# Performance work log

Hardware: AMD Instinct MI355X
Metric: run time of the kernel (lower is better)

## Reference

```python
import jax, jax.numpy as jnp
import numpy as np

N_LAYERS = 4
NA = 64    # n_processor_a
NB = 64    # n_processor_b
NP = NA + NB
M = 32     # N_modes
HA = 512   # fine grid resolution
HB = 128   # coarse grid resolution
N_IN_A = 4
N_IN_B = 4
N_OUT_A = 2


def setup_inputs() -> dict:
    key = jax.random.key(0)
    ks = jax.random.split(key, 16)
    def w(k, shape, fan_in):
        return jax.random.normal(k, shape, jnp.float32) * (fan_in ** -0.5)
    return {
        "u_a": jax.random.normal(ks[0], (2, HA, HA), jnp.float32),
        "x_a": jax.random.normal(ks[1], (2, HA, HA), jnp.float32),
        "u_b": jax.random.normal(ks[2], (2, HB, HB), jnp.float32),
        "x_b": jax.random.normal(ks[3], (2, HB, HB), jnp.float32),
        "enc_a_w": w(ks[4], (NA, N_IN_A), N_IN_A),
        "enc_a_b": jnp.zeros((NA,), jnp.float32),
        "enc_b_w": w(ks[5], (NB, N_IN_B), N_IN_B),
        "enc_b_b": jnp.zeros((NB,), jnp.float32),
        "dec_w": w(ks[6], (N_OUT_A, NA), NA),
        "dec_b": jnp.zeros((N_OUT_A,), jnp.float32),
        "c1a_w": w(ks[7], (N_LAYERS, NA, NA), NA),
        "c1a_b": jnp.zeros((N_LAYERS, NA), jnp.float32),
        "c2a_w": w(ks[8], (N_LAYERS, NA, NA), NA),
        "c2a_b": jnp.zeros((N_LAYERS, NA), jnp.float32),
        "c1b_w": w(ks[9], (N_LAYERS - 1, NB, NB), NB),
        "c1b_b": jnp.zeros((N_LAYERS - 1, NB), jnp.float32),
        "c2b_w": w(ks[10], (N_LAYERS - 1, NB, NB), NB),
        "c2b_b": jnp.zeros((N_LAYERS - 1, NB), jnp.float32),
        "A_re": jax.random.normal(ks[11], (N_LAYERS, NP, NP, M, M), jnp.float32) * 0.02,
        "A_im": jax.random.normal(ks[12], (N_LAYERS, NP, NP, M, M), jnp.float32) * 0.02,
    }


def conv1x1(w, b, x):
    # w: [out,in], b: [out], x: [in,H,W] -> [out,H,W]
    return jnp.einsum('oi,ihw->ohw', w, x) + b[:, None, None]


def rfft2_truncate(x, m):
    # x: [C,H,W] real -> [C,m,m] complex (forward-normalized, centered rows)
    c = jnp.fft.rfft2(x, norm='forward')[:, :, :m]
    return jnp.roll(c, m // 2, axis=1)[:, :m]


def irfft2_pad(c, m, s):
    # c: [C,m,m] complex -> [C,*s] real
    c = jnp.pad(c, ((0, 0), (0, s[0] - c.shape[1]), (0, s[1] - c.shape[2])))
    c = jnp.roll(c, -(m // 2), axis=1)
    return jnp.fft.irfft2(c, s=s, norm='forward')


def biscale_spectral_conv(ua, ub, Wc):
    m = Wc.shape[-1]
    coeff = jnp.concatenate([rfft2_truncate(ua, m), rfft2_truncate(ub, m)], axis=0)
    coeff = jnp.einsum('oimn,imn->omn', Wc, coeff)  # complex channel mixing per mode
    na = ua.shape[0]
    out1 = irfft2_pad(coeff[:na], m, ua.shape[1:])
    out2 = irfft2_pad(coeff[na:], m, ub.shape[1:])
    return out1, out2


def _forward(u_a, x_a, u_b, x_b, enc_a_w, enc_a_b, enc_b_w, enc_b_b, dec_w, dec_b,
             c1a_w, c1a_b, c2a_w, c2a_b, c1b_w, c1b_b, c2b_w, c2b_b, A_re, A_im):
    A = A_re + 1j * A_im  # [L, NP, NP, M, M] complex64
    ua = conv1x1(enc_a_w, enc_a_b, jnp.concatenate([x_a, u_a], 0))
    ub = conv1x1(enc_b_w, enc_b_b, jnp.concatenate([x_b, u_b], 0))
    n_layers_b = c1b_w.shape[0]
    for i in range(A.shape[0]):
        ua_, ub_ = biscale_spectral_conv(ua, ub, A[i])
        ua = ua + jax.nn.gelu(conv1x1(c2a_w[i], c2a_b[i],
                                      jax.nn.gelu(conv1x1(c1a_w[i], c1a_b[i], ua_))))
        if i != n_layers_b:
            ub = ub + jax.nn.gelu(conv1x1(c2b_w[i], c2b_b[i],
                                          jax.nn.gelu(conv1x1(c1b_w[i], c1b_b[i], ub_))))
    ua = conv1x1(dec_w, dec_b, ua)
    return (ua, ub)


def reference(u_a, x_a, u_b, x_b, enc_a_w, enc_a_b, enc_b_w, enc_b_b, dec_w, dec_b,
              c1a_w, c1a_b, c2a_w, c2a_b, c1b_w, c1b_b, c2b_w, c2b_b, A_re, A_im):
    return _forward(u_a, x_a, u_b, x_b, enc_a_w, enc_a_b, enc_b_w, enc_b_b, dec_w, dec_b,
                    c1a_w, c1a_b, c2a_w, c2a_b, c1b_w, c1b_b, c2b_w, c2b_b, A_re, A_im)
```

## Files before the change

kernel.cpp:

```cpp
#include <hip/hip_runtime.h>
#include <hip/hip_bf16.h>
#include <math.h>


__device__ __forceinline__ float gelu_f(float x) {
  float t = tanhf(0.7978845608028654f * (x + 0.044715f * x * x * x));
  return 0.5f * x * (1.0f + t);
}

__device__ __forceinline__ float2 cmulf(float2 a, float2 b) {
  return make_float2(a.x * b.x - a.y * b.y, a.x * b.y + a.y * b.x);
}

__global__ void ktab(float2* __restrict__ t512) {
  int k = blockIdx.x * 256 + threadIdx.x;
  if (k < 512) {
    float a = (float)((double)k * (6.283185307179586 / 512.0));
    t512[k] = make_float2(cosf(a), sinf(a));
  }
}

template <int HW>
__global__ __launch_bounds__(256) void kenc(const float* __restrict__ xin,
                                            const float* __restrict__ uin,
                                            const float* __restrict__ w,
                                            const float* __restrict__ b,
                                            float* __restrict__ out) {
  int p = blockIdx.x * 256 + threadIdx.x;
  float i0 = xin[p], i1 = xin[HW + p];
  float i2 = uin[p], i3 = uin[HW + p];
  for (int c = 0; c < 64; ++c)
    out[(size_t)c * HW + p] =
        w[c * 4 + 0] * i0 + w[c * 4 + 1] * i1 + w[c * 4 + 2] * i2 + w[c * 4 + 3] * i3 + b[c];
}

template <int H, int MUL>
__global__ __launch_bounds__(256) void kfwd1(const float* __restrict__ x, float2* __restrict__ G,
                                             const float2* __restrict__ tw, float fs) {
  constexpr int PAD = H + 8;
  __shared__ float sm[8 * PAD];
  int c = blockIdx.x / (H / 8);
  int h8 = blockIdx.x % (H / 8);
  const float* src = x + ((size_t)c * H + h8 * 8) * H;
  for (int i = threadIdx.x; i < 2 * H; i += 256) {
    float4 g = ((const float4*)src)[i];
    int r = (i * 4) >> (H == 512 ? 9 : 7);
    int col = (i * 4) & (H - 1);
    *(float4*)&sm[r * PAD + col] = g;
  }
  __syncthreads();
  int kc = threadIdx.x >> 3;
  int hl = threadIdx.x & 7;
  float2 w0 = tw[(kc * MUL) & 511];
  float twoc = 2.f * w0.x;
  const float* row = sm + hl * PAD;
  float v1 = 0.f, v2 = 0.f;
#pragma unroll 4
  for (int w = 0; w < H; w += 2) {
    v2 = fmaf(twoc, v1, row[w] - v2);
    v1 = fmaf(twoc, v2, row[w + 1] - v1);
  }
  int h = h8 * 8 + hl;
  G[((size_t)c * 32 + kc) * H + h] =
      make_float2(fs * fmaf(w0.x, v1, -v2), fs * (w0.y * v1));
}

template <int H, int MUL>
__global__ __launch_bounds__(256) void kfwd2(const float2* __restrict__ G, float2* __restrict__ coeff,
                                             const float2* __restrict__ tw, int cbase) {
  __shared__ float2 gs[H];
  int c = blockIdx.x >> 5, kc = blockIdx.x & 31;
  const float2* gr = G + ((size_t)c * 32 + kc) * H;
  for (int i = threadIdx.x; i < H; i += 256) gs[i] = gr[i];
  __syncthreads();
  int jr = threadIdx.x >> 3, sub = threadIdx.x & 7;
  int f = jr - 16;
  float2 cur = tw[(f * sub * MUL) & 511];
  float2 step = tw[(f * 8 * MUL) & 511];
  float re = 0.f, im = 0.f;
  for (int j = 0; j < H / 8; ++j) {
    float2 g = gs[sub + 8 * j];
    re += g.x * cur.x + g.y * cur.y;
    im += g.y * cur.x - g.x * cur.y;
    cur = cmulf(cur, step);
  }
  for (int d = 1; d < 8; d <<= 1) {
    re += __shfl_down(re, d, 8);
    im += __shfl_down(im, d, 8);
  }
  if (sub == 0) coeff[(size_t)(cbase + c) * 1024 + jr * 32 + kc] = make_float2(re, im);
}

__global__ __launch_bounds__(256) void kmix(const float* __restrict__ Are,
                                            const float* __restrict__ Aim,
                                            const float2* __restrict__ cin,
                                            float2* __restrict__ cout) {
  int idx = blockIdx.x * 256 + threadIdx.x;
  int mn = idx & 1023;
  int o = idx >> 10;
  const float* ar = Are + (size_t)o * 131072 + mn;
  const float* ai = Aim + (size_t)o * 131072 + mn;
  float re = 0.f, im = 0.f;
  for (int i = 0; i < 128; ++i) {
    float wr = ar[(size_t)i * 1024];
    float wi = ai[(size_t)i * 1024];
    float2 x = cin[(size_t)i * 1024 + mn];
    re += wr * x.x - wi * x.y;
    im += wr * x.y + wi * x.x;
  }
  cout[(size_t)o * 1024 + mn] = make_float2(re, im);
}

template <int H, int MUL>
__global__ __launch_bounds__(256) void kinv1(const float2* __restrict__ coeff, float2* __restrict__ T,
                                             const float2* __restrict__ tw, int cbase) {
  __shared__ float2 cs[1024];
  int c = blockIdx.x / (H / 8);
  int h8 = blockIdx.x % (H / 8);
  const float2* cr = coeff + (size_t)(cbase + c) * 1024;
  for (int i = threadIdx.x; i < 1024; i += 256) cs[i] = cr[i];
  __syncthreads();
  int kc = threadIdx.x & 31;
  int hl = threadIdx.x >> 5;
  int h = h8 * 8 + hl;
  float2 cur = tw[((-16) * h * MUL) & 511];
  float2 step = tw[(h * MUL) & 511];
  float re = 0.f, im = 0.f;
  for (int jr = 0; jr < 32; ++jr) {
    float2 x = cs[jr * 32 + kc];
    re += x.x * cur.x - x.y * cur.y;
    im += x.x * cur.y + x.y * cur.x;
    cur = cmulf(cur, step);
  }
  float wgt = (kc == 0) ? 1.f : 2.f;
  T[((size_t)c * H + h) * 32 + kc] = make_float2(re * wgt, im * wgt);
}

template <int H, int MUL, int RPB>
__global__ __launch_bounds__(256) void kinv2(const float2* __restrict__ T, float* __restrict__ out,
                                             const float2* __restrict__ tw) {
  constexpr int QW = H / 4;
  __shared__ float2 ts[RPB * 32];
  size_t row0 = (size_t)blockIdx.x * RPB;
  for (int i = threadIdx.x; i < RPB * 32; i += 256) ts[i] = T[row0 * 32 + i];
  __syncthreads();
  int r = threadIdx.x / QW;
  int w0 = threadIdx.x % QW;
  float2 b = tw[(w0 * MUL) & 511];
  float2 c = make_float2(1.f, 0.f);
  float a0 = 0.f, a1 = 0.f, a2 = 0.f, a3 = 0.f;
  const float2* tr = &ts[r * 32];
#pragma unroll
  for (int kc = 0; kc < 32; kc += 4) {
    float2 t0 = tr[kc];
    float zre = t0.x * c.x - t0.y * c.y;
    a0 += zre; a1 += zre; a2 += zre; a3 += zre;
    c = cmulf(c, b);
    t0 = tr[kc + 1];
    zre = t0.x * c.x - t0.y * c.y;
    float zim = t0.x * c.y + t0.y * c.x;
    a0 += zre; a1 -= zim; a2 -= zre; a3 += zim;
    c = cmulf(c, b);
    t0 = tr[kc + 2];
    zre = t0.x * c.x - t0.y * c.y;
    a0 += zre; a1 -= zre; a2 += zre; a3 -= zre;
    c = cmulf(c, b);
    t0 = tr[kc + 3];
    zre = t0.x * c.x - t0.y * c.y;
    zim = t0.x * c.y + t0.y * c.x;
    a0 += zre; a1 += zim; a2 -= zre; a3 -= zim;
    c = cmulf(c, b);
  }
  float* orow = out + (row0 + r) * H + w0;
  orow[0] = a0;
  orow[QW] = a1;
  orow[2 * QW] = a2;
  orow[3 * QW] = a3;
}

template <int HW>
__global__ __launch_bounds__(256) void kconv(const float* __restrict__ xin, float* __restrict__ uio,
                                             const float* __restrict__ w1, const float* __restrict__ b1,
                                             const float* __restrict__ w2, const float* __restrict__ b2) {
  __shared__ float Xs[64][65];
  __shared__ float Ws[64][65];
  int p0 = blockIdx.x * 64;
  int t = threadIdx.x;
  for (int i = t; i < 4096; i += 256) {
    int r = i >> 6, cidx = i & 63;
    Xs[r][cidx] = xin[(size_t)r * HW + p0 + cidx];
    Ws[r][cidx] = w1[i];
  }
  __syncthreads();
  int ocb = (t >> 4) * 4;
  int pb = (t & 15) * 4;
  float acc[16];
#pragma unroll
  for (int i = 0; i < 4; ++i) {
    float bi = b1[ocb + i];
#pragma unroll
    for (int j = 0; j < 4; ++j) acc[i * 4 + j] = bi;
  }
  for (int ci = 0; ci < 64; ++ci) {
    float a0 = Ws[ocb + 0][ci], a1 = Ws[ocb + 1][ci], a2 = Ws[ocb + 2][ci], a3 = Ws[ocb + 3][ci];
    float x0 = Xs[ci][pb + 0], x1 = Xs[ci][pb + 1], x2 = Xs[ci][pb + 2], x3 = Xs[ci][pb + 3];
    acc[0] = fmaf(a0, x0, acc[0]); acc[1] = fmaf(a0, x1, acc[1]);
    acc[2] = fmaf(a0, x2, acc[2]); acc[3] = fmaf(a0, x3, acc[3]);
    acc[4] = fmaf(a1, x0, acc[4]); acc[5] = fmaf(a1, x1, acc[5]);
    acc[6] = fmaf(a1, x2, acc[6]); acc[7] = fmaf(a1, x3, acc[7]);
    acc[8] = fmaf(a2, x0, acc[8]); acc[9] = fmaf(a2, x1, acc[9]);
    acc[10] = fmaf(a2, x2, acc[10]); acc[11] = fmaf(a2, x3, acc[11]);
    acc[12] = fmaf(a3, x0, acc[12]); acc[13] = fmaf(a3, x1, acc[13]);
    acc[14] = fmaf(a3, x2, acc[14]); acc[15] = fmaf(a3, x3, acc[15]);
  }
  __syncthreads();
#pragma unroll
  for (int i = 0; i < 4; ++i)
#pragma unroll
    for (int j = 0; j < 4; ++j) Xs[ocb + i][pb + j] = gelu_f(acc[i * 4 + j]);
  for (int i = t; i < 4096; i += 256) Ws[i >> 6][i & 63] = w2[i];
  __syncthreads();
#pragma unroll
  for (int i = 0; i < 4; ++i) {
    float bi = b2[ocb + i];
#pragma unroll
    for (int j = 0; j < 4; ++j) acc[i * 4 + j] = bi;
  }
  for (int ci = 0; ci < 64; ++ci) {
    float a0 = Ws[ocb + 0][ci], a1 = Ws[ocb + 1][ci], a2 = Ws[ocb + 2][ci], a3 = Ws[ocb + 3][ci];
    float x0 = Xs[ci][pb + 0], x1 = Xs[ci][pb + 1], x2 = Xs[ci][pb + 2], x3 = Xs[ci][pb + 3];
    acc[0] = fmaf(a0, x0, acc[0]); acc[1] = fmaf(a0, x1, acc[1]);
    acc[2] = fmaf(a0, x2, acc[2]); acc[3] = fmaf(a0, x3, acc[3]);
    acc[4] = fmaf(a1, x0, acc[4]); acc[5] = fmaf(a1, x1, acc[5]);
    acc[6] = fmaf(a1, x2, acc[6]); acc[7] = fmaf(a1, x3, acc[7]);
    acc[8] = fmaf(a2, x0, acc[8]); acc[9] = fmaf(a2, x1, acc[9]);
    acc[10] = fmaf(a2, x2, acc[10]); acc[11] = fmaf(a2, x3, acc[11]);
    acc[12] = fmaf(a3, x0, acc[12]); acc[13] = fmaf(a3, x1, acc[13]);
    acc[14] = fmaf(a3, x2, acc[14]); acc[15] = fmaf(a3, x3, acc[15]);
  }
#pragma unroll
  for (int i = 0; i < 4; ++i) {
    float4* dst = (float4*)&uio[(size_t)(ocb + i) * HW + p0 + pb];
    float4 u = *dst;
    u.x += gelu_f(acc[i * 4 + 0]);
    u.y += gelu_f(acc[i * 4 + 1]);
    u.z += gelu_f(acc[i * 4 + 2]);
    u.w += gelu_f(acc[i * 4 + 3]);
    *dst = u;
  }
}

__global__ __launch_bounds__(256) void kdecf(const float* __restrict__ ua, const float* __restrict__ w,
                                             const float* __restrict__ b, float* __restrict__ out) {
  int p = blockIdx.x * 256 + threadIdx.x;
  float a0 = b[0], a1 = b[1];
  for (int c = 0; c < 64; ++c) {
    float xv = ua[(size_t)c * 262144 + p];
    a0 = fmaf(w[c], xv, a0);
    a1 = fmaf(w[64 + c], xv, a1);
  }
  out[p] = a0;
  out[262144 + p] = a1;
}

__global__ __launch_bounds__(256) void kcopyf(const float* __restrict__ src, float* __restrict__ out) {
  int p = blockIdx.x * 256 + threadIdx.x;
  out[p] = src[p];
}

extern "C" void kernel_launch(void* const* d_in, const int* in_sizes, int n_in,
                              void* d_out, int out_size, void* d_ws, size_t ws_size,
                              hipStream_t stream) {
  (void)in_sizes; (void)n_in; (void)out_size;
  const float* u_a = (const float*)d_in[0];
  const float* x_a = (const float*)d_in[1];
  const float* u_b = (const float*)d_in[2];
  const float* x_b = (const float*)d_in[3];
  const float* enc_a_w = (const float*)d_in[4];
  const float* enc_a_b = (const float*)d_in[5];
  const float* enc_b_w = (const float*)d_in[6];
  const float* enc_b_b = (const float*)d_in[7];
  const float* dec_w = (const float*)d_in[8];
  const float* dec_b = (const float*)d_in[9];
  const float* c1a_w = (const float*)d_in[10];
  const float* c1a_b = (const float*)d_in[11];
  const float* c2a_w = (const float*)d_in[12];
  const float* c2a_b = (const float*)d_in[13];
  const float* c1b_w = (const float*)d_in[14];
  const float* c1b_b = (const float*)d_in[15];
  const float* c2b_w = (const float*)d_in[16];
  const float* c2b_b = (const float*)d_in[17];
  const float* A_re = (const float*)d_in[18];
  const float* A_im = (const float*)d_in[19];

  if (ws_size < (size_t)38798336 * 4) return;

  float* F = (float*)d_ws;
  float* ua = F;
  float* ua_ = F + 16777216;
  float* ub = F + 33554432;
  float* ub_ = F + 34603008;
  float2* GTa = (float2*)(F + 35651584);
  float2* GTb = (float2*)(F + 37748736);
  float2* coef = (float2*)(F + 38273024);
  float2* coef2 = (float2*)(F + 38535168);
  float2* t512 = (float2*)(F + 38797312);
  float* out = (float*)d_out;

  ktab<<<2, 256, 0, stream>>>(t512);

  const float FA = 1.f / 262144.f, FB = 1.f / 16384.f;
  kenc<262144><<<1024, 256, 0, stream>>>(x_a, u_a, enc_a_w, enc_a_b, ua);
  kenc<16384><<<64, 256, 0, stream>>>(x_b, u_b, enc_b_w, enc_b_b, ub);
  for (int l = 0; l < 4; ++l) {
    kfwd1<512, 1><<<4096, 256, 0, stream>>>(ua, GTa, t512, FA);
    kfwd2<512, 1><<<2048, 256, 0, stream>>>(GTa, coef, t512, 0);
    kfwd1<128, 4><<<1024, 256, 0, stream>>>(ub, GTb, t512, FB);
    kfwd2<128, 4><<<2048, 256, 0, stream>>>(GTb, coef, t512, 64);
    int nout = (l < 3) ? 128 : 64;
    kmix<<<nout * 4, 256, 0, stream>>>(A_re + (size_t)l * 16777216,
                                       A_im + (size_t)l * 16777216, coef, coef2);
    kinv1<512, 1><<<4096, 256, 0, stream>>>(coef2, GTa, t512, 0);
    kinv2<512, 1, 2><<<16384, 256, 0, stream>>>(GTa, ua_, t512);
    kconv<262144><<<4096, 256, 0, stream>>>(ua_, ua, c1a_w + l * 4096, c1a_b + l * 64,
                                            c2a_w + l * 4096, c2a_b + l * 64);
    if (l < 3) {
      kinv1<128, 4><<<1024, 256, 0, stream>>>(coef2, GTb, t512, 64);
      kinv2<128, 4, 8><<<1024, 256, 0, stream>>>(GTb, ub_, t512);
      kconv<16384><<<256, 256, 0, stream>>>(ub_, ub, c1b_w + l * 4096, c1b_b + l * 64,
                                            c2b_w + l * 4096, c2b_b + l * 64);
    }
  }

  kdecf<<<1024, 256, 0, stream>>>(ua, dec_w, dec_b, out);
  kcopyf<<<4096, 256, 0, stream>>>(ub, out + 524288);
}
```

Baseline: 991.9 us.

## Fuse inverse row DFT into the pointwise MLP conv kernel

Merges the second inverse-DFT stage (kinv2) into the 1x1-conv MLP kernel. Each block computes the 64 spatial outputs of its row segment for all 64 channels directly from the 32 truncated row coefficients in shared memory. This removes a full-resolution intermediate write and read (ua_/ub_, 64 MB for the fine grid) per layer, plus one kernel launch. The cost is a less efficient in-block inverse DFT without the quarter-wave symmetry trick, more shared memory per block, and more strided loads of the spectral input.

```diff
diff --git a/kernel.cpp b/kernel.cpp
--- a/kernel.cpp
+++ b/kernel.cpp
@@ -136,73 +136,79 @@
   T[((size_t)c * H + h) * 32 + kc] = make_float2(re * wgt, im * wgt);
 }
 
-template <int H, int MUL, int RPB>
-__global__ __launch_bounds__(256) void kinv2(const float2* __restrict__ T, float* __restrict__ out,
-                                             const float2* __restrict__ tw) {
-  constexpr int QW = H / 4;
-  __shared__ float2 ts[RPB * 32];
-  size_t row0 = (size_t)blockIdx.x * RPB;
-  for (int i = threadIdx.x; i < RPB * 32; i += 256) ts[i] = T[row0 * 32 + i];
-  __syncthreads();
-  int r = threadIdx.x / QW;
-  int w0 = threadIdx.x % QW;
-  float2 b = tw[(w0 * MUL) & 511];
-  float2 c = make_float2(1.f, 0.f);
-  float a0 = 0.f, a1 = 0.f, a2 = 0.f, a3 = 0.f;
-  const float2* tr = &ts[r * 32];
-#pragma unroll
-  for (int kc = 0; kc < 32; kc += 4) {
-    float2 t0 = tr[kc];
-    float zre = t0.x * c.x - t0.y * c.y;
-    a0 += zre; a1 += zre; a2 += zre; a3 += zre;
-    c = cmulf(c, b);
-    t0 = tr[kc + 1];
-    zre = t0.x * c.x - t0.y * c.y;
-    float zim = t0.x * c.y + t0.y * c.x;
-    a0 += zre; a1 -= zim; a2 -= zre; a3 += zim;
-    c = cmulf(c, b);
-    t0 = tr[kc + 2];
-    zre = t0.x * c.x - t0.y * c.y;
-    a0 += zre; a1 -= zre; a2 += zre; a3 -= zre;
-    c = cmulf(c, b);
-    t0 = tr[kc + 3];
-    zre = t0.x * c.x - t0.y * c.y;
-    zim = t0.x * c.y + t0.y * c.x;
-    a0 += zre; a1 += zim; a2 -= zre; a3 -= zim;
-    c = cmulf(c, b);
-  }
-  float* orow = out + (row0 + r) * H + w0;
-  orow[0] = a0;
-  orow[QW] = a1;
-  orow[2 * QW] = a2;
-  orow[3 * QW] = a3;
-}
-
-template <int HW>
-__global__ __launch_bounds__(256) void kconv(const float* __restrict__ xin, float* __restrict__ uio,
-                                             const float* __restrict__ w1, const float* __restrict__ b1,
-                                             const float* __restrict__ w2, const float* __restrict__ b2) {
+template <int H, int MUL, int HW>
+__global__ __launch_bounds__(256) void kinvconv(const float2* __restrict__ T,
+                                                float* __restrict__ uio,
+                                                const float* __restrict__ w1,
+                                                const float* __restrict__ b1,
+                                                const float* __restrict__ w2,
+                                                const float* __restrict__ b2,
+                                                const float2* __restrict__ tw) {
+  __shared__ float2 Ts[2048];
   __shared__ float Xs[64][65];
   __shared__ float Ws[64][65];
   int p0 = blockIdx.x * 64;
+  int h = p0 / H;
+  int w0 = p0 % H;
   int t = threadIdx.x;
-  for (int i = t; i < 4096; i += 256) {
-    int r = i >> 6, cidx = i & 63;
-    Xs[r][cidx] = xin[(size_t)r * HW + p0 + cidx];
-    Ws[r][cidx] = w1[i];
-  }
-  __syncthreads();
-  int ocb = (t >> 4) * 4;
+  for (int i = t; i < 2048; i += 256) {
+    int c = i >> 5, kc = i & 31;
+    Ts[i] = T[((size_t)c * H + h) * 32 + kc];
+  }
+  for (int i = t; i < 4096; i += 256) Ws[i >> 6][i & 63] = w1[i];
+  __syncthreads();
+  int cb = (t >> 4) * 4;
   int pb = (t & 15) * 4;
   float acc[16];
+  {
+    float2 s0 = tw[((w0 + pb + 0) * MUL) & 511];
+    float2 s1 = tw[((w0 + pb + 1) * MUL) & 511];
+    float2 s2 = tw[((w0 + pb + 2) * MUL) & 511];
+    float2 s3 = tw[((w0 + pb + 3) * MUL) & 511];
+    float2 c0 = make_float2(1.f, 0.f), c1 = c0, c2 = c0, c3 = c0;
+#pragma unroll
+    for (int i = 0; i < 16; ++i) acc[i] = 0.f;
+    const float2* t0 = &Ts[(cb + 0) * 32];
+    const float2* t1 = &Ts[(cb + 1) * 32];
+    const float2* t2 = &Ts[(cb + 2) * 32];
+    const float2* t3 = &Ts[(cb + 3) * 32];
+    for (int kc = 0; kc < 32; ++kc) {
+      float2 v0 = t0[kc], v1 = t1[kc], v2 = t2[kc], v3 = t3[kc];
+      acc[0] += v0.x * c0.x - v0.y * c0.y;
+      acc[1] += v0.x * c1.x - v0.y * c1.y;
+      acc[2] += v0.x * c2.x - v0.y * c2.y;
+      acc[3] += v0.x * c3.x - v0.y * c3.y;
+      acc[4] += v1.x * c0.x - v1.y * c0.y;
+      acc[5] += v1.x * c1.x - v1.y * c1.y;
+      acc[6] += v1.x * c2.x - v1.y * c2.y;
+      acc[7] += v1.x * c3.x - v1.y * c3.y;
+      acc[8] += v2.x * c0.x - v2.y * c0.y;
+      acc[9] += v2.x * c1.x - v2.y * c1.y;
+      acc[10] += v2.x * c2.x - v2.y * c2.y;
+      acc[11] += v2.x * c3.x - v2.y * c3.y;
+      acc[12] += v3.x * c0.x - v3.y * c0.y;
+      acc[13] += v3.x * c1.x - v3.y * c1.y;
+      acc[14] += v3.x * c2.x - v3.y * c2.y;
+      acc[15] += v3.x * c3.x - v3.y * c3.y;
+      c0 = cmulf(c0, s0);
+      c1 = cmulf(c1, s1);
+      c2 = cmulf(c2, s2);
+      c3 = cmulf(c3, s3);
+    }
+#pragma unroll
+    for (int i = 0; i < 4; ++i)
+#pragma unroll
+      for (int j = 0; j < 4; ++j) Xs[cb + i][pb + j] = acc[i * 4 + j];
+  }
+  __syncthreads();
 #pragma unroll
   for (int i = 0; i < 4; ++i) {
-    float bi = b1[ocb + i];
+    float bi = b1[cb + i];
 #pragma unroll
     for (int j = 0; j < 4; ++j) acc[i * 4 + j] = bi;
   }
   for (int ci = 0; ci < 64; ++ci) {
-    float a0 = Ws[ocb + 0][ci], a1 = Ws[ocb + 1][ci], a2 = Ws[ocb + 2][ci], a3 = Ws[ocb + 3][ci];
+    float a0 = Ws[cb + 0][ci], a1 = Ws[cb + 1][ci], a2 = Ws[cb + 2][ci], a3 = Ws[cb + 3][ci];
     float x0 = Xs[ci][pb + 0], x1 = Xs[ci][pb + 1], x2 = Xs[ci][pb + 2], x3 = Xs[ci][pb + 3];
     acc[0] = fmaf(a0, x0, acc[0]); acc[1] = fmaf(a0, x1, acc[1]);
     acc[2] = fmaf(a0, x2, acc[2]); acc[3] = fmaf(a0, x3, acc[3]);
@@ -217,17 +223,17 @@
 #pragma unroll
   for (int i = 0; i < 4; ++i)
 #pragma unroll
-    for (int j = 0; j < 4; ++j) Xs[ocb + i][pb + j] = gelu_f(acc[i * 4 + j]);
+    for (int j = 0; j < 4; ++j) Xs[cb + i][pb + j] = gelu_f(acc[i * 4 + j]);
   for (int i = t; i < 4096; i += 256) Ws[i >> 6][i & 63] = w2[i];
   __syncthreads();
 #pragma unroll
   for (int i = 0; i < 4; ++i) {
-    float bi = b2[ocb + i];
+    float bi = b2[cb + i];
 #pragma unroll
     for (int j = 0; j < 4; ++j) acc[i * 4 + j] = bi;
   }
   for (int ci = 0; ci < 64; ++ci) {
-    float a0 = Ws[ocb + 0][ci], a1 = Ws[ocb + 1][ci], a2 = Ws[ocb + 2][ci], a3 = Ws[ocb + 3][ci];
+    float a0 = Ws[cb + 0][ci], a1 = Ws[cb + 1][ci], a2 = Ws[cb + 2][ci], a3 = Ws[cb + 3][ci];
     float x0 = Xs[ci][pb + 0], x1 = Xs[ci][pb + 1], x2 = Xs[ci][pb + 2], x3 = Xs[ci][pb + 3];
     acc[0] = fmaf(a0, x0, acc[0]); acc[1] = fmaf(a0, x1, acc[1]);
     acc[2] = fmaf(a0, x2, acc[2]); acc[3] = fmaf(a0, x3, acc[3]);
@@ -240,7 +246,7 @@
   }
 #pragma unroll
   for (int i = 0; i < 4; ++i) {
-    float4* dst = (float4*)&uio[(size_t)(ocb + i) * HW + p0 + pb];
+    float4* dst = (float4*)&uio[(size_t)(cb + i) * HW + p0 + pb];
     float4 u = *dst;
     u.x += gelu_f(acc[i * 4 + 0]);
     u.y += gelu_f(acc[i * 4 + 1]);
@@ -297,9 +303,7 @@
 
   float* F = (float*)d_ws;
   float* ua = F;
-  float* ua_ = F + 16777216;
   float* ub = F + 33554432;
-  float* ub_ = F + 34603008;
   float2* GTa = (float2*)(F + 35651584);
   float2* GTb = (float2*)(F + 37748736);
   float2* coef = (float2*)(F + 38273024);
@@ -321,14 +325,14 @@
     kmix<<<nout * 4, 256, 0, stream>>>(A_re + (size_t)l * 16777216,
                                        A_im + (size_t)l * 16777216, coef, coef2);
     kinv1<512, 1><<<4096, 256, 0, stream>>>(coef2, GTa, t512, 0);
-    kinv2<512, 1, 2><<<16384, 256, 0, stream>>>(GTa, ua_, t512);
-    kconv<262144><<<4096, 256, 0, stream>>>(ua_, ua, c1a_w + l * 4096, c1a_b + l * 64,
-                                            c2a_w + l * 4096, c2a_b + l * 64);
+    kinvconv<512, 1, 262144><<<4096, 256, 0, stream>>>(GTa, ua, c1a_w + l * 4096,
+                                                       c1a_b + l * 64, c2a_w + l * 4096,
+                                                       c2a_b + l * 64, t512);
     if (l < 3) {
       kinv1<128, 4><<<1024, 256, 0, stream>>>(coef2, GTb, t512, 64);
-      kinv2<128, 4, 8><<<1024, 256, 0, stream>>>(GTb, ub_, t512);
-      kconv<16384><<<256, 256, 0, stream>>>(ub_, ub, c1b_w + l * 4096, c1b_b + l * 64,
-                                            c2b_w + l * 4096, c2b_b + l * 64);
+      kinvconv<128, 4, 16384><<<256, 256, 0, stream>>>(GTb, ub, c1b_w + l * 4096,
+                                                       c1b_b + l * 64, c2b_w + l * 4096,
+                                                       c2b_b + l * 64, t512);
     }
   }
 
```

New measurement: 1.056 ms. 6.5% more time.
